# Kernel optimization log

Hardware: AMD Instinct MI355X
Metric: run time of the kernel (lower is better)

The kernel has to match this reference:

```python
import jax, jax.numpy as jnp
import numpy as np

B, M, A = 64, 16, 128
H = 128            # cfg.SUB.DIM
P = 16             # NUM_PHYSICOCHEMICAL
NUM_ATOM_TYPES = 100
NUM_FP_TYPES = 2048
EPS_W = 1e-8
EPS_LN = 1e-5


def setup_inputs() -> dict:
    key = jax.random.key(0)
    ks = jax.random.split(key, 16)
    def xavier(k, shape):
        fan_in, fan_out = shape[0], shape[-1]
        lim = float(np.sqrt(6.0 / (fan_in + fan_out)))
        return jax.random.uniform(k, shape, jnp.float32, -lim, lim)
    return {
        "atom_features": jax.random.randint(ks[0], (B, M, A), 0, NUM_ATOM_TYPES),
        "fingerprints": jax.random.randint(ks[1], (B, M, A), 0, NUM_FP_TYPES),
        "phys": jax.random.normal(ks[2], (B, M, P), jnp.float32),
        "ratios": jax.random.uniform(ks[3], (B, M), jnp.float32),
        # learned params
        "atom_emb": xavier(ks[4], (NUM_ATOM_TYPES, H)),
        "fp_emb": xavier(ks[5], (NUM_FP_TYPES, H)),
        "W_in": xavier(ks[6], (2 * H, H)),
        "b_in": jnp.zeros((H,), jnp.float32),
        "ln_g": jnp.ones((H + P,), jnp.float32),
        "ln_b": jnp.zeros((H + P,), jnp.float32),
        "W1": xavier(ks[7], (H + P, H)),
        "b1": jnp.zeros((H,), jnp.float32),
        "W2": xavier(ks[8], (H, 1)),
        "b2": jnp.zeros((1,), jnp.float32),
    }


def reference(atom_features, fingerprints, phys, ratios,
              atom_emb, fp_emb, W_in, b_in, ln_g, ln_b, W1, b1, W2, b2):
    # per-molecule embed: gather both tables, concat, linear, relu, mean over atoms
    e = jnp.concatenate([atom_emb[atom_features], fp_emb[fingerprints]], axis=-1)  # [B,M,A,2H]
    h = jax.nn.relu(jnp.einsum('bmad,dh->bmah', e, W_in) + b_in)                   # [B,M,A,H]
    mol = h.mean(axis=2)                                                           # [B,M,H]

    pv = jnp.nan_to_num(phys, nan=0.0, posinf=1000.0, neginf=-1000.0)              # [B,M,P]

    # normalized mixing weights per batch item
    w = ratios / (ratios.sum(axis=1, keepdims=True) + EPS_W)                       # [B,M]
    mix_h = jnp.einsum('bm,bmh->bh', w, mol)                                       # [B,H]
    mix_p = jnp.einsum('bm,bmp->bp', w, pv)                                        # [B,P]

    z = jnp.concatenate([mix_h, mix_p], axis=-1)                                   # [B,H+P]
    # head: LayerNorm -> Linear -> ReLU -> Linear (dropout p=0, eval)
    mu = z.mean(axis=-1, keepdims=True)
    var = ((z - mu) ** 2).mean(axis=-1, keepdims=True)
    zn = (z - mu) / jnp.sqrt(var + EPS_LN) * ln_g + ln_b
    y = jax.nn.relu(zn @ W1 + b1) @ W2 + b2                                        # [B,1]
    return jnp.nan_to_num(y)
```

## Files before the change

### kernel.cpp

```cpp
#include <hip/hip_runtime.h>
#include <math.h>
#include <float.h>

#define B_ 64
#define M_ 16
#define A_ 128
#define H_ 128
#define P_ 16
#define NAT 100
#define NFP 2048
#define ZDIM (H_ + P_)

__device__ float g_Ta[NAT * H_];
__device__ float g_Tf[NFP * H_];
__device__ float g_mol[B_ * M_ * H_];

#define K1_BLOCKS (NAT / 4 + NFP / 4)
__global__ __launch_bounds__(128)
void k1_precompute(const float* __restrict__ atom_emb,
                   const float* __restrict__ fp_emb,
                   const float* __restrict__ W_in) {
    __shared__ float e[4][H_];
    const int j = threadIdx.x;
    const float* emb; const float* W; float* out; int base;
    if (blockIdx.x < NAT / 4) {
        base = blockIdx.x * 4;           emb = atom_emb; W = W_in;            out = g_Ta;
    } else {
        base = (blockIdx.x - NAT / 4) * 4; emb = fp_emb;  W = W_in + H_ * H_; out = g_Tf;
    }
#pragma unroll
    for (int r = 0; r < 4; ++r) e[r][j] = emb[(base + r) * H_ + j];
    __syncthreads();
    float a0 = 0.f, a1 = 0.f, a2 = 0.f, a3 = 0.f;
#pragma unroll 8
    for (int k = 0; k < H_; ++k) {
        const float wk = W[k * H_ + j];
        a0 += e[0][k] * wk;
        a1 += e[1][k] * wk;
        a2 += e[2][k] * wk;
        a3 += e[3][k] * wk;
    }
    out[(base + 0) * H_ + j] = a0;
    out[(base + 1) * H_ + j] = a1;
    out[(base + 2) * H_ + j] = a2;
    out[(base + 3) * H_ + j] = a3;
}

__global__ __launch_bounds__(128)
void k2_mol(const int* __restrict__ af, const int* __restrict__ fpi,
            const float* __restrict__ b_in) {
    __shared__ int ia[A_];
    __shared__ int ifp[A_];
    __shared__ float sh[4][H_];
    const int bm = blockIdx.x, t = threadIdx.x;
    const int q = t & 31, s = t >> 5;
    ia[t]  = af[bm * A_ + t];
    ifp[t] = fpi[bm * A_ + t];
    __syncthreads();
    const float4 bj = *(const float4*)&b_in[4 * q];
    float4 acc = make_float4(0.f, 0.f, 0.f, 0.f);
#pragma unroll 8
    for (int a = s; a < A_; a += 4) {
        const int ra = ia[a], rf = ifp[a];
        const float4 va = *(const float4*)&g_Ta[ra * H_ + 4 * q];
        const float4 vf = *(const float4*)&g_Tf[rf * H_ + 4 * q];
        acc.x += fmaxf(va.x + vf.x + bj.x, 0.f);
        acc.y += fmaxf(va.y + vf.y + bj.y, 0.f);
        acc.z += fmaxf(va.z + vf.z + bj.z, 0.f);
        acc.w += fmaxf(va.w + vf.w + bj.w, 0.f);
    }
    *(float4*)&sh[s][4 * q] = acc;
    __syncthreads();
    const int j = t;
    g_mol[bm * H_ + j] =
        (sh[0][j] + sh[1][j] + sh[2][j] + sh[3][j]) * (1.0f / (float)A_);
}

__global__ __launch_bounds__(128)
void k3_head(const float* __restrict__ phys,
             const float* __restrict__ ratios,
             const float* __restrict__ ln_g,
             const float* __restrict__ ln_b,
             const float* __restrict__ W1,
             const float* __restrict__ b1,
             const float* __restrict__ W2,
             const float* __restrict__ b2,
             float* __restrict__ out) {
    const int b = blockIdx.x, j = threadIdx.x;
    __shared__ float w[M_];
    __shared__ float z[ZDIM];
    __shared__ float zn[ZDIM];
    __shared__ float red[H_];

    if (j < M_) w[j] = ratios[b * M_ + j];
    __syncthreads();

    float rsum = 0.f;
#pragma unroll
    for (int m = 0; m < M_; ++m) rsum += w[m];
    const float dinv = 1.0f / (rsum + 1e-8f);

    float acc = 0.f;
#pragma unroll
    for (int m = 0; m < M_; ++m) acc += (w[m] * dinv) * g_mol[(b * M_ + m) * H_ + j];
    z[j] = acc;

    if (j < P_) {
        float accp = 0.f;
#pragma unroll
        for (int m = 0; m < M_; ++m) {
            float pv = phys[(b * M_ + m) * P_ + j];
            if (isnan(pv)) pv = 0.f;
            else if (isinf(pv)) pv = (pv > 0.f) ? 1000.f : -1000.f;
            accp += (w[m] * dinv) * pv;
        }
        z[H_ + j] = accp;
    }
    __syncthreads();

    float s = 0.f;
#pragma unroll 8
    for (int k = 0; k < ZDIM; ++k) s += z[k];
    const float mu = s * (1.0f / (float)ZDIM);
    float s2 = 0.f;
#pragma unroll 8
    for (int k = 0; k < ZDIM; ++k) { float d = z[k] - mu; s2 += d * d; }
    const float rstd = rsqrtf(s2 * (1.0f / (float)ZDIM) + 1e-5f);

    for (int k = j; k < ZDIM; k += H_)
        zn[k] = (z[k] - mu) * rstd * ln_g[k] + ln_b[k];
    __syncthreads();

    float a1 = 0.f;
#pragma unroll 8
    for (int k = 0; k < ZDIM; ++k) a1 += zn[k] * W1[k * H_ + j];
    const float h1 = fmaxf(a1 + b1[j], 0.f);
    red[j] = h1 * W2[j];
    __syncthreads();

    if (j == 0) {
        float y = b2[0];
#pragma unroll 8
        for (int k = 0; k < H_; ++k) y += red[k];
        if (isnan(y)) y = 0.f;
        else if (isinf(y)) y = (y > 0.f) ? FLT_MAX : -FLT_MAX;
        out[b] = y;
    }
}

extern "C" void kernel_launch(void* const* d_in, const int* in_sizes, int n_in,
                              void* d_out, int out_size, void* d_ws, size_t ws_size,
                              hipStream_t stream) {
    const int*   af    = (const int*)d_in[0];
    const int*   fpi   = (const int*)d_in[1];
    const float* phys  = (const float*)d_in[2];
    const float* ratio = (const float*)d_in[3];
    const float* aemb  = (const float*)d_in[4];
    const float* femb  = (const float*)d_in[5];
    const float* W_in  = (const float*)d_in[6];
    const float* b_in  = (const float*)d_in[7];
    const float* ln_g  = (const float*)d_in[8];
    const float* ln_b  = (const float*)d_in[9];
    const float* W1    = (const float*)d_in[10];
    const float* b1    = (const float*)d_in[11];
    const float* W2    = (const float*)d_in[12];
    const float* b2    = (const float*)d_in[13];
    float* out = (float*)d_out;

    k1_precompute<<<dim3(K1_BLOCKS), dim3(H_), 0, stream>>>(aemb, femb, W_in);
    k2_mol<<<dim3(B_ * M_), dim3(H_), 0, stream>>>(af, fpi, b_in);
    k3_head<<<dim3(B_), dim3(H_), 0, stream>>>(phys, ratio, ln_g, ln_b, W1, b1, W2, b2, out);
}
```

Measured before the change: 108.3 us.

## Fuse three kernels into one cooperative kernel with grid-wide syncs

Replaces the three separate launches (table precompute, per-molecule gather-mean, head) with one cooperative kernel of 512 blocks × 256 threads that separates the phases with grid.sync(). The aim is to remove launch gaps and inter-kernel overhead. Work per block is regrouped: 8 rows per block for the precompute, and two molecules per block with 8 atom-strided lanes for the gather. It falls back to the old three-kernel path if cooperative launch is unavailable or fails. Grid syncs cost something, and the head phase keeps only 64 blocks busy.

```diff
diff --git a/kernel.cpp b/kernel.cpp
--- a/kernel.cpp
+++ b/kernel.cpp
@@ -1,6 +1,9 @@
 #include <hip/hip_runtime.h>
+#include <hip/hip_cooperative_groups.h>
 #include <math.h>
 #include <float.h>
+
+namespace cg = cooperative_groups;
 
 #define B_ 64
 #define M_ 16
@@ -11,9 +14,157 @@
 #define NFP 2048
 #define ZDIM (H_ + P_)
 
+#define FUSED_BLOCKS 512
+#define FUSED_THREADS 256
+#define NROWGROUPS 269
+
 __device__ float g_Ta[NAT * H_];
 __device__ float g_Tf[NFP * H_];
 __device__ float g_mol[B_ * M_ * H_];
+
+__global__ __launch_bounds__(FUSED_THREADS)
+void fused_all(const int* __restrict__ af, const int* __restrict__ fpi,
+               const float* __restrict__ phys, const float* __restrict__ ratios,
+               const float* __restrict__ aemb, const float* __restrict__ femb,
+               const float* __restrict__ W_in, const float* __restrict__ b_in,
+               const float* __restrict__ ln_g, const float* __restrict__ ln_b,
+               const float* __restrict__ W1, const float* __restrict__ b1,
+               const float* __restrict__ W2, const float* __restrict__ b2,
+               float* __restrict__ out) {
+    cg::grid_group grid = cg::this_grid();
+    const int t = threadIdx.x;
+
+    __shared__ float e8[8][H_];
+    __shared__ int   ia[A_];
+    __shared__ int   ifp[A_];
+    __shared__ float sh8[8][H_];
+    __shared__ float wr[M_];
+    __shared__ float z[ZDIM];
+    __shared__ float zn[ZDIM];
+    __shared__ float red[H_];
+
+    {
+        const int g = blockIdx.x;
+        if (g < NROWGROUPS) {
+            const int j = t & (H_ - 1);
+            const int half = t >> 7;
+            const float* emb; const float* W; float* outT; int nrows; int base;
+            if (g < 13) { base = g * 8;        emb = aemb; W = W_in;            outT = g_Ta; nrows = NAT; }
+            else        { base = (g - 13) * 8; emb = femb; W = W_in + H_ * H_;  outT = g_Tf; nrows = NFP; }
+            const int r0 = base + half * 4;
+#pragma unroll
+            for (int i = 0; i < 4; ++i) {
+                const int r = r0 + i;
+                e8[half * 4 + i][j] = (r < nrows) ? emb[r * H_ + j] : 0.f;
+            }
+            __syncthreads();
+            float a0 = 0.f, a1 = 0.f, a2 = 0.f, a3 = 0.f;
+#pragma unroll 8
+            for (int k = 0; k < H_; ++k) {
+                const float wk = W[k * H_ + j];
+                a0 += e8[half * 4 + 0][k] * wk;
+                a1 += e8[half * 4 + 1][k] * wk;
+                a2 += e8[half * 4 + 2][k] * wk;
+                a3 += e8[half * 4 + 3][k] * wk;
+            }
+            if (r0 + 0 < nrows) outT[(r0 + 0) * H_ + j] = a0;
+            if (r0 + 1 < nrows) outT[(r0 + 1) * H_ + j] = a1;
+            if (r0 + 2 < nrows) outT[(r0 + 2) * H_ + j] = a2;
+            if (r0 + 3 < nrows) outT[(r0 + 3) * H_ + j] = a3;
+        }
+    }
+    grid.sync();
+
+    {
+        const int q = t & 31, s = t >> 5;
+        const float4 bj = *(const float4*)&b_in[4 * q];
+#pragma unroll
+        for (int it = 0; it < 2; ++it) {
+            const int bm = blockIdx.x * 2 + it;
+            if (t < A_) { ia[t] = af[bm * A_ + t]; ifp[t] = fpi[bm * A_ + t]; }
+            __syncthreads();
+            float4 acc = make_float4(0.f, 0.f, 0.f, 0.f);
+#pragma unroll 8
+            for (int a = s; a < A_; a += 8) {
+                const int ra = ia[a], rf = ifp[a];
+                const float4 va = *(const float4*)&g_Ta[ra * H_ + 4 * q];
+                const float4 vf = *(const float4*)&g_Tf[rf * H_ + 4 * q];
+                acc.x += fmaxf(va.x + vf.x + bj.x, 0.f);
+                acc.y += fmaxf(va.y + vf.y + bj.y, 0.f);
+                acc.z += fmaxf(va.z + vf.z + bj.z, 0.f);
+                acc.w += fmaxf(va.w + vf.w + bj.w, 0.f);
+            }
+            *(float4*)&sh8[s][4 * q] = acc;
+            __syncthreads();
+            if (t < H_) {
+                const float m = sh8[0][t] + sh8[1][t] + sh8[2][t] + sh8[3][t]
+                              + sh8[4][t] + sh8[5][t] + sh8[6][t] + sh8[7][t];
+                g_mol[bm * H_ + t] = m * (1.0f / (float)A_);
+            }
+            __syncthreads();
+        }
+    }
+    grid.sync();
+
+    if (blockIdx.x < B_) {
+        const int b = blockIdx.x;
+        const int j = t;
+        if (t < M_) wr[t] = ratios[b * M_ + t];
+        __syncthreads();
+        if (t < H_) {
+            float rsum = 0.f;
+#pragma unroll
+            for (int m = 0; m < M_; ++m) rsum += wr[m];
+            const float dinv = 1.0f / (rsum + 1e-8f);
+            float acc = 0.f;
+#pragma unroll
+            for (int m = 0; m < M_; ++m)
+                acc += (wr[m] * dinv) * g_mol[(b * M_ + m) * H_ + j];
+            z[j] = acc;
+            if (j < P_) {
+                float accp = 0.f;
+#pragma unroll
+                for (int m = 0; m < M_; ++m) {
+                    float pv = phys[(b * M_ + m) * P_ + j];
+                    if (isnan(pv)) pv = 0.f;
+                    else if (isinf(pv)) pv = (pv > 0.f) ? 1000.f : -1000.f;
+                    accp += (wr[m] * dinv) * pv;
+                }
+                z[H_ + j] = accp;
+            }
+        }
+        __syncthreads();
+        if (t < H_) {
+            float sm = 0.f;
+#pragma unroll 8
+            for (int k = 0; k < ZDIM; ++k) sm += z[k];
+            const float mu = sm * (1.0f / (float)ZDIM);
+            float s2 = 0.f;
+#pragma unroll 8
+            for (int k = 0; k < ZDIM; ++k) { const float d = z[k] - mu; s2 += d * d; }
+            const float rstd = rsqrtf(s2 * (1.0f / (float)ZDIM) + 1e-5f);
+            for (int k = j; k < ZDIM; k += H_)
+                zn[k] = (z[k] - mu) * rstd * ln_g[k] + ln_b[k];
+        }
+        __syncthreads();
+        if (t < H_) {
+            float a1v = 0.f;
+#pragma unroll 8
+            for (int k = 0; k < ZDIM; ++k) a1v += zn[k] * W1[k * H_ + j];
+            const float h1 = fmaxf(a1v + b1[j], 0.f);
+            red[j] = h1 * W2[j];
+        }
+        __syncthreads();
+        if (t == 0) {
+            float y = b2[0];
+#pragma unroll 8
+            for (int k = 0; k < H_; ++k) y += red[k];
+            if (isnan(y)) y = 0.f;
+            else if (isinf(y)) y = (y > 0.f) ? FLT_MAX : -FLT_MAX;
+            out[b] = y;
+        }
+    }
+}
 
 #define K1_BLOCKS (NAT / 4 + NFP / 4)
 __global__ __launch_bounds__(128)
@@ -24,9 +175,9 @@
     const int j = threadIdx.x;
     const float* emb; const float* W; float* out; int base;
     if (blockIdx.x < NAT / 4) {
-        base = blockIdx.x * 4;           emb = atom_emb; W = W_in;            out = g_Ta;
+        base = blockIdx.x * 4;             emb = atom_emb; W = W_in;            out = g_Ta;
     } else {
-        base = (blockIdx.x - NAT / 4) * 4; emb = fp_emb;  W = W_in + H_ * H_; out = g_Tf;
+        base = (blockIdx.x - NAT / 4) * 4; emb = fp_emb;   W = W_in + H_ * H_;  out = g_Tf;
     }
 #pragma unroll
     for (int r = 0; r < 4; ++r) e[r][j] = emb[(base + r) * H_ + j];
@@ -151,6 +302,7 @@
 extern "C" void kernel_launch(void* const* d_in, const int* in_sizes, int n_in,
                               void* d_out, int out_size, void* d_ws, size_t ws_size,
                               hipStream_t stream) {
+    (void)in_sizes; (void)n_in; (void)out_size; (void)d_ws; (void)ws_size;
     const int*   af    = (const int*)d_in[0];
     const int*   fpi   = (const int*)d_in[1];
     const float* phys  = (const float*)d_in[2];
@@ -167,6 +319,24 @@
     const float* b2    = (const float*)d_in[13];
     float* out = (float*)d_out;
 
+    static int coop = -1;
+    if (coop < 0) {
+        int dev = 0, v = 0;
+        hipGetDevice(&dev);
+        if (hipDeviceGetAttribute(&v, hipDeviceAttributeCooperativeLaunch, dev) != hipSuccess)
+            v = 0;
+        coop = v;
+    }
+
+    if (coop) {
+        void* args[] = { &af, &fpi, &phys, &ratio, &aemb, &femb, &W_in, &b_in,
+                         &ln_g, &ln_b, &W1, &b1, &W2, &b2, &out };
+        hipError_t rc = hipLaunchCooperativeKernel(
+            fused_all, dim3(FUSED_BLOCKS), dim3(FUSED_THREADS), args, 0u, stream);
+        if (rc == hipSuccess) return;
+        coop = 0;
+    }
+
     k1_precompute<<<dim3(K1_BLOCKS), dim3(H_), 0, stream>>>(aemb, femb, W_in);
     k2_mol<<<dim3(B_ * M_), dim3(H_), 0, stream>>>(af, fpi, b_in);
     k3_head<<<dim3(B_), dim3(H_), 0, stream>>>(phys, ratio, ln_g, ln_b, W1, b1, W2, b2, out);
```

Result: slower. 232.7 us (+114.8%).
